# Optimization experiments

Hardware: AMD Instinct MI355X
Metric: run time of the kernel (lower is better)

## Reference

```python
import jax, jax.numpy as jnp
import numpy as np

SR = 16000
BLOCK_SIZE = 160
N_WT = 64
WT_LEN = 512
SEC = 60
T = SR * SEC  # 960000 samples
FRAMES = 100 * SEC  # 6000 attention frames


def _make_sine_table(length, cycle, phase):
    i = np.arange(length, dtype=np.float32)
    wt = np.sin(cycle * 2 * np.pi * i / length + 2 * phase * np.pi).astype(np.float32)
    wt[-1] = wt[0]  # loop-closing trick: last sample = first sample
    return wt


def setup_inputs() -> dict:
    key = jax.random.key(0)
    k1, k2, k3, k4 = jax.random.split(key, 4)
    pitch = jax.random.uniform(k1, (1, T, 1), dtype=jnp.float32) * 360.0 + 40.0  # 40..400 Hz
    amplitude = jax.random.uniform(k2, (1, T, 1), dtype=jnp.float32)
    # wavetables: first 4 are fixed sine harmonics with wrapped endpoint, rest learned
    rng = np.random.default_rng(0)
    wts = np.asarray(jax.random.normal(k3, (N_WT, WT_LEN), dtype=jnp.float32)) * 0.01
    for idx in range(4):
        wts[idx] = _make_sine_table(WT_LEN, idx + 1, rng.uniform(0.0, 1.0))
    wts[4:, -1] = wts[4:, 0]  # wrap endpoint for learned tables too
    attention = jax.random.normal(k4, (N_WT, FRAMES), dtype=jnp.float32)
    return {
        "pitch": pitch,
        "amplitude": amplitude,
        "wavetables": jnp.asarray(wts),
        "attention": attention,
        "sec": SEC,
    }


def reference(pitch, amplitude, wavetables, attention, sec):
    L = wavetables.shape[1]
    freq = pitch.reshape(-1)  # [T], torch .squeeze()
    inc = freq / SR * L  # phase increment per sample
    # exclusive cumulative sum: cumsum(inc) - inc  (matches cumsum - increment[0] broadcast)
    idx = (jnp.cumsum(inc) - inc) % L  # [T]
    lo = jnp.floor(idx)
    hi = jnp.ceil(idx)
    alpha = idx - lo  # fractional part
    lo_i = lo.astype(jnp.int32)
    hi_i = hi.astype(jnp.int32) % L
    # tanh applied to learned tables (idx >= 4); fixed sine tables passed through
    wts_eff = jnp.concatenate([wavetables[:4], jnp.tanh(wavetables[4:])], axis=0)  # [64, L]
    w_lo = wts_eff[:, lo_i]  # [64, T] gather
    w_hi = wts_eff[:, hi_i]  # [64, T] gather
    osc = w_lo + alpha[None, :] * (w_hi - w_lo)  # [64, T] linear interp
    att = jax.nn.softmax(attention, axis=0)  # softmax over wavetables
    att_up = jnp.repeat(att, BLOCK_SIZE, axis=1)  # nearest-neighbor upsample -> [64, T]
    mixed = jnp.sum(osc * att_up, axis=0)  # [T]
    return mixed[None, :, None] * amplitude  # [1, T, 1]
```

## Files before the change

kernel.cpp:

```cpp
#include <hip/hip_runtime.h>
#include <math.h>

#define BLKSZ 160
#define NWT   64
#define WTLEN 512
#define FPB   16
#define SPB   2560

#define NB1   3750
#define NB1P  3760
#define NB2   235
#define NB2P  240
#define NB3   15

static __device__ __forceinline__ float inc32_of(float p) {
    return (p / 16000.0f) * 512.0f;
}

__global__ __launch_bounds__(256) void k_leaf(
    const float* __restrict__ pitch, const float* __restrict__ wts,
    float* __restrict__ bs1, float* __restrict__ wts_eff, int T)
{
    int t = threadIdx.x;
    if (blockIdx.x >= NB2) {
        int i = (blockIdx.x - NB2) * 256 + t;
        if (i < NWT * WTLEN) {
            float v = wts[i];
            if ((i >> 9) >= 4) v = tanhf(v);
            wts_eff[i] = v;
        }
        return;
    }
    __shared__ float b0[256];
    int blk = blockIdx.x;
    size_t s0 = (size_t)blk * 4096;
    int nsamp = min(4096, T - (int)s0);
    int nb0 = nsamp >> 4;
    if (t < nb0) {
        const float4* p4 = (const float4*)(pitch + s0 + (size_t)t * 16);
        float acc = 0.f;
        #pragma unroll
        for (int i = 0; i < 4; ++i) {
            float4 v = p4[i];
            acc = acc + inc32_of(v.x);
            acc = acc + inc32_of(v.y);
            acc = acc + inc32_of(v.z);
            acc = acc + inc32_of(v.w);
        }
        b0[t] = acc;
    }
    __syncthreads();
    int nb1 = nb0 >> 4;
    if (t < nb1) {
        float acc = b0[t * 16];
        for (int j = 1; j < 16; ++j) acc = acc + b0[t * 16 + j];
        bs1[blk * 16 + t] = acc;
    }
}

__global__ __launch_bounds__(512) void k_main(
    const float* __restrict__ pitch, const float* __restrict__ amp,
    const float* __restrict__ att, const float* __restrict__ wts_eff,
    const float* __restrict__ bs1g, float* __restrict__ out, int frames)
{
    __shared__ float sm[FPB][NWT];
    __shared__ float mixrow[FPB][WTLEN];
    __shared__ float pr[SPB];
    __shared__ float roffL[SPB / 16];
    __shared__ float bs2L[NB2P];
    __shared__ float bs3L[NB3];
    __shared__ float S4L[NB3];
    __shared__ float S3w[2];
    __shared__ float S2w[11];
    __shared__ float bs1prevL;

    float* bs1L = &mixrow[0][0];

    int tid = threadIdx.x, lane = tid & 63, wv = tid >> 6;
    int b = blockIdx.x;
    int f0 = b * FPB;
    size_t base = (size_t)b * SPB;
    int j0 = 10 * b - 2;
    int rlo = max(j0, 0) >> 4;

    #pragma unroll
    for (int r = 0; r < 2; ++r) {
        int f = f0 + wv * 2 + r;
        float a = att[(size_t)lane * frames + f];
        float m = a;
        #pragma unroll
        for (int off = 32; off; off >>= 1) m = fmaxf(m, __shfl_xor(m, off, 64));
        float e = expf(a - m);
        float s = e;
        #pragma unroll
        for (int off = 32; off; off >>= 1) s += __shfl_xor(s, off, 64);
        sm[wv * 2 + r][lane] = e / s;
    }

    float increg[SPB / 512];
    #pragma unroll
    for (int i = 0; i < SPB / 512; ++i) {
        increg[i] = inc32_of(pitch[base + i * 512 + tid]);
        pr[i * 512 + tid] = increg[i];
    }
    for (int i = tid; i < NB1P; i += 512)
        bs1L[i] = (i < NB1) ? bs1g[i] : 0.f;
    __syncthreads();

    if (tid < SPB / 16) {
        int bofs = tid * 16;
        float acc = pr[bofs];
        for (int j = 1; j < 16; ++j) { acc = acc + pr[bofs + j]; pr[bofs + j] = acc; }
    }
    if (tid >= 272 && tid < 272 + NB2P) {
        int t2 = tid - 272;
        float a = 0.f;
        if (t2 < NB2) {
            a = bs1L[t2 * 16];
            for (int j = 1; j < 16; ++j) a = a + bs1L[t2 * 16 + j];
        }
        bs2L[t2] = a;
    }
    __syncthreads();
    if (tid < NB3) {
        float a = bs2L[tid * 16];
        for (int j = 1; j < 16; ++j) a = a + bs2L[tid * 16 + j];
        bs3L[tid] = a;
    }
    __syncthreads();
    if (tid == 0) {
        float a = 0.f;
        for (int i = 0; i < NB3; ++i) { a = a + bs3L[i]; S4L[i] = a; }
    }
    __syncthreads();
    if (tid < 2) {
        int r = rlo - 1 + tid;
        float v = 0.f;
        if (r >= 0 && r < NB2) {
            int g = r >> 4, p = r & 15;
            float a = bs2L[g * 16];
            for (int k = 1; k <= p; ++k) a = a + bs2L[g * 16 + k];
            v = g ? (a + S4L[g - 1]) : a;
        }
        S3w[tid] = v;
    }
    if (tid == 2) bs1prevL = (b > 0) ? bs1L[10 * b - 1] : 0.f;
    __syncthreads();
    if (tid < 11) {
        int j = j0 + tid;
        float v = 0.f;
        if (j >= 0) {
            int r = j >> 4, p = j & 15;
            float a = bs1L[r * 16];
            for (int q = 1; q <= p; ++q) a = a + bs1L[r * 16 + q];
            v = r ? (a + S3w[r - rlo]) : a;
        }
        S2w[tid] = v;
    }
    __syncthreads();

    if (tid < SPB / 16) {
        float v;
        if (tid == 0) {
            v = (b == 0) ? 0.f : (bs1prevL + S2w[0]);
        } else {
            int lr = (tid - 1) >> 4;
            int p  = (tid - 1) & 15;
            float acc = pr[(lr * 16) * 16 + 15];
            for (int q = 1; q <= p; ++q) acc = acc + pr[(lr * 16 + q) * 16 + 15];
            int gr = 10 * b + lr;
            v = gr ? (acc + S2w[lr + 1]) : acc;
        }
        roffL[tid] = v;
    }
    {
        float acc[FPB];
        #pragma unroll
        for (int k = 0; k < FPB; ++k) acc[k] = 0.f;
        for (int w = 0; w < NWT; ++w) {
            float v = wts_eff[w * WTLEN + tid];
            #pragma unroll
            for (int k = 0; k < FPB; ++k) acc[k] += sm[k][w] * v;
        }
        #pragma unroll
        for (int k = 0; k < FPB; ++k) mixrow[k][tid] = acc[k];
    }
    __syncthreads();

    #pragma unroll
    for (int i = 0; i < SPB / 512; ++i) {
        int tl = i * 512 + tid;
        size_t tg = base + tl;
        float C = pr[tl] + roffL[tl >> 4];
        float sub = C - increg[i];
        float idx = fmodf(sub, 512.0f);
        if (idx < 0.f) idx += 512.f;
        int li = (int)idx;
        float alpha = idx - (float)li;
        int hi = ((int)ceilf(idx)) & (WTLEN - 1);
        int fr = tl / BLKSZ;
        float wlo = mixrow[fr][li];
        float whi = mixrow[fr][hi];
        out[tg] = (wlo + alpha * (whi - wlo)) * amp[tg];
    }
}

extern "C" void kernel_launch(void* const* d_in, const int* in_sizes, int n_in,
                              void* d_out, int out_size, void* d_ws, size_t ws_size,
                              hipStream_t stream) {
    const float* pitch = (const float*)d_in[0];
    const float* amp   = (const float*)d_in[1];
    const float* wts   = (const float*)d_in[2];
    const float* att   = (const float*)d_in[3];

    int T      = in_sizes[0];
    int frames = T / BLKSZ;
    int nmain  = T / SPB;

    float* ws      = (float*)d_ws;
    float* wts_eff = ws;
    float* bs1     = ws + 32768;
    float* out     = (float*)d_out;

    int nwts_blocks = (NWT * WTLEN + 255) / 256;
    k_leaf<<<NB2 + nwts_blocks, 256, 0, stream>>>(pitch, wts, bs1, wts_eff, T);
    k_main<<<nmain, 512, 0, stream>>>(pitch, amp, att, wts_eff, bs1, out, frames);
}
```

Measured before the change: 28.53 us.

## Enlarge main-kernel tile to 24 frames with 768 threads and transposed softmax

Each main block now covers 24 attention frames (3840 samples) with 768 threads instead of 16 frames with 512. That gives 250 blocks, which fit in a single wave across the CUs instead of a 1.5-wave tail. The mixed-wavetable build is redistributed so each thread computes 8 frames for two table positions. It reads softmax weights from a transposed shared array with float4 loads, and the prefix-offset indexing is adjusted for the larger tile. The trade-off is more shared memory and registers per block, and fewer blocks to hide latency.

New measurement: 25.57 us. -10.4%, faster.

```diff
diff --git a/kernel.cpp b/kernel.cpp
--- a/kernel.cpp
+++ b/kernel.cpp
@@ -4,8 +4,10 @@
 #define BLKSZ 160
 #define NWT   64
 #define WTLEN 512
-#define FPB   16
-#define SPB   2560
+#define FPB   24
+#define SPB   3840
+#define NTHR  768
+#define SMP   28
 
 #define NB1   3750
 #define NB1P  3760
@@ -58,12 +60,12 @@
     }
 }
 
-__global__ __launch_bounds__(512) void k_main(
+__global__ __launch_bounds__(768, 3) void k_main(
     const float* __restrict__ pitch, const float* __restrict__ amp,
     const float* __restrict__ att, const float* __restrict__ wts_eff,
     const float* __restrict__ bs1g, float* __restrict__ out, int frames)
 {
-    __shared__ float sm[FPB][NWT];
+    __shared__ float smT[NWT][SMP];
     __shared__ float mixrow[FPB][WTLEN];
     __shared__ float pr[SPB];
     __shared__ float roffL[SPB / 16];
@@ -71,7 +73,7 @@
     __shared__ float bs3L[NB3];
     __shared__ float S4L[NB3];
     __shared__ float S3w[2];
-    __shared__ float S2w[11];
+    __shared__ float S2w[16];
     __shared__ float bs1prevL;
 
     float* bs1L = &mixrow[0][0];
@@ -80,7 +82,7 @@
     int b = blockIdx.x;
     int f0 = b * FPB;
     size_t base = (size_t)b * SPB;
-    int j0 = 10 * b - 2;
+    int j0 = 15 * b - 2;
     int rlo = max(j0, 0) >> 4;
 
     #pragma unroll
@@ -94,16 +96,16 @@
         float s = e;
         #pragma unroll
         for (int off = 32; off; off >>= 1) s += __shfl_xor(s, off, 64);
-        sm[wv * 2 + r][lane] = e / s;
-    }
-
-    float increg[SPB / 512];
+        smT[lane][wv * 2 + r] = e / s;
+    }
+
+    float increg[SPB / NTHR];
     #pragma unroll
-    for (int i = 0; i < SPB / 512; ++i) {
-        increg[i] = inc32_of(pitch[base + i * 512 + tid]);
-        pr[i * 512 + tid] = increg[i];
-    }
-    for (int i = tid; i < NB1P; i += 512)
+    for (int i = 0; i < SPB / NTHR; ++i) {
+        increg[i] = inc32_of(pitch[base + i * NTHR + tid]);
+        pr[i * NTHR + tid] = increg[i];
+    }
+    for (int i = tid; i < NB1P; i += NTHR)
         bs1L[i] = (i < NB1) ? bs1g[i] : 0.f;
     __syncthreads();
 
@@ -144,9 +146,9 @@
         }
         S3w[tid] = v;
     }
-    if (tid == 2) bs1prevL = (b > 0) ? bs1L[10 * b - 1] : 0.f;
-    __syncthreads();
-    if (tid < 11) {
+    if (tid == 2) bs1prevL = (b > 0) ? bs1L[15 * b - 1] : 0.f;
+    __syncthreads();
+    if (tid < 16) {
         int j = j0 + tid;
         float v = 0.f;
         if (j >= 0) {
@@ -168,28 +170,38 @@
             int p  = (tid - 1) & 15;
             float acc = pr[(lr * 16) * 16 + 15];
             for (int q = 1; q <= p; ++q) acc = acc + pr[(lr * 16 + q) * 16 + 15];
-            int gr = 10 * b + lr;
+            int gr = 15 * b + lr;
             v = gr ? (acc + S2w[lr + 1]) : acc;
         }
         roffL[tid] = v;
     }
     {
-        float acc[FPB];
-        #pragma unroll
-        for (int k = 0; k < FPB; ++k) acc[k] = 0.f;
-        for (int w = 0; w < NWT; ++w) {
-            float v = wts_eff[w * WTLEN + tid];
+        #pragma unroll
+        for (int it = 0; it < 2; ++it) {
+            int item = tid + it * NTHR;
+            int fg = item >> 9;
+            int j  = item & 511;
+            float acc[8];
             #pragma unroll
-            for (int k = 0; k < FPB; ++k) acc[k] += sm[k][w] * v;
-        }
-        #pragma unroll
-        for (int k = 0; k < FPB; ++k) mixrow[k][tid] = acc[k];
+            for (int k = 0; k < 8; ++k) acc[k] = 0.f;
+            for (int w = 0; w < NWT; ++w) {
+                float v = wts_eff[w * WTLEN + j];
+                float4 s0 = *(const float4*)&smT[w][fg * 8];
+                float4 s1 = *(const float4*)&smT[w][fg * 8 + 4];
+                acc[0] += s0.x * v;  acc[1] += s0.y * v;
+                acc[2] += s0.z * v;  acc[3] += s0.w * v;
+                acc[4] += s1.x * v;  acc[5] += s1.y * v;
+                acc[6] += s1.z * v;  acc[7] += s1.w * v;
+            }
+            #pragma unroll
+            for (int k = 0; k < 8; ++k) mixrow[fg * 8 + k][j] = acc[k];
+        }
     }
     __syncthreads();
 
     #pragma unroll
-    for (int i = 0; i < SPB / 512; ++i) {
-        int tl = i * 512 + tid;
+    for (int i = 0; i < SPB / NTHR; ++i) {
+        int tl = i * NTHR + tid;
         size_t tg = base + tl;
         float C = pr[tl] + roffL[tl >> 4];
         float sub = C - increg[i];
@@ -224,5 +236,5 @@
 
     int nwts_blocks = (NWT * WTLEN + 255) / 256;
     k_leaf<<<NB2 + nwts_blocks, 256, 0, stream>>>(pitch, wts, bs1, wts_eff, T);
-    k_main<<<nmain, 512, 0, stream>>>(pitch, amp, att, wts_eff, bs1, out, frames);
-}
+    k_main<<<nmain, 768, 0, stream>>>(pitch, amp, att, wts_eff, bs1, out, frames);
+}
```
